# Kernel optimization log

Measured on AMD Instinct MI355X. Metric: run time of the kernel, lower is better.

## Reference

```python
import jax, jax.numpy as jnp
import numpy as np

DIM = 512
HEADS = 8
HEAD_DIM = DIM // HEADS
WIN = 7
GC = DIM // 4
EPS = 1e-5


def dwconv1d(x, w, b):
    # x: (B, Cg, L), w: (Cg, 1, k) depthwise, b: (Cg,)
    k = w.shape[-1]
    out = jax.lax.conv_general_dilated(
        x, w, window_strides=(1,), padding=[(k // 2, k // 2)],
        dimension_numbers=("NCH", "OIH", "NCH"), feature_group_count=x.shape[1])
    return out + b[None, :, None]


def group_norm(x, groups, w, b):
    # x: (B, C, *spatial); normalize over (C//groups, *spatial) per group
    shp = x.shape
    xg = x.reshape(shp[0], groups, -1)
    mu = xg.mean(-1, keepdims=True)
    var = xg.var(-1, keepdims=True)
    xn = ((xg - mu) / jnp.sqrt(var + EPS)).reshape(shp)
    bshape = (1, shp[1]) + (1,) * (x.ndim - 2)
    return xn * w.reshape(bshape) + b.reshape(bshape)


def setup_inputs() -> dict:
    key = jax.random.key(0)
    ks = jax.random.split(key, 16)
    inp = {
        "x": jax.random.normal(ks[0], (32, DIM, 56, 56), dtype=jnp.float32),
        "w3": jax.random.normal(ks[1], (GC, 1, 3), dtype=jnp.float32) * 0.2,
        "b3": jax.random.normal(ks[2], (GC,), dtype=jnp.float32) * 0.02,
        "w5": jax.random.normal(ks[3], (GC, 1, 5), dtype=jnp.float32) * 0.2,
        "b5": jax.random.normal(ks[4], (GC,), dtype=jnp.float32) * 0.02,
        "w7": jax.random.normal(ks[5], (GC, 1, 7), dtype=jnp.float32) * 0.2,
        "b7": jax.random.normal(ks[6], (GC,), dtype=jnp.float32) * 0.02,
        "w9": jax.random.normal(ks[7], (GC, 1, 9), dtype=jnp.float32) * 0.2,
        "b9": jax.random.normal(ks[8], (GC,), dtype=jnp.float32) * 0.02,
        "gnh_w": jnp.ones((DIM,), jnp.float32),
        "gnh_b": jnp.zeros((DIM,), jnp.float32),
        "gnw_w": jnp.ones((DIM,), jnp.float32),
        "gnw_b": jnp.zeros((DIM,), jnp.float32),
        "gn_w": jnp.ones((DIM,), jnp.float32),
        "gn_b": jnp.zeros((DIM,), jnp.float32),
        "qw": jax.random.normal(ks[9], (DIM,), dtype=jnp.float32) * 0.2,
        "kw": jax.random.normal(ks[10], (DIM,), dtype=jnp.float32) * 0.2,
        "vw": jax.random.normal(ks[11], (DIM,), dtype=jnp.float32) * 0.2,
    }
    return inp


def reference(x, w3, b3, w5, b5, w7, b7, w9, b9,
              gnh_w, gnh_b, gnw_w, gnw_b, gn_w, gn_b, qw, kw, vw):
    B, C, H, W = x.shape
    ws = [(w3, b3), (w5, b5), (w7, b7), (w9, b9)]

    def multi_dwc(xp):  # xp: (B, C, L)
        parts = jnp.split(xp, 4, axis=1)
        return jnp.concatenate([dwconv1d(p, w, b) for p, (w, b) in zip(parts, ws)], axis=1)

    x_h = x.mean(axis=3)  # (B, C, H)
    x_w = x.mean(axis=2)  # (B, C, W)
    x_h_attn = jax.nn.sigmoid(group_norm(multi_dwc(x_h), 4, gnh_w, gnh_b))  # (B,C,H)
    x_w_attn = jax.nn.sigmoid(group_norm(multi_dwc(x_w), 4, gnw_w, gnw_b))  # (B,C,W)
    xg = x * x_h_attn[:, :, :, None] * x_w_attn[:, :, None, :]

    # avg-pool downsample by window_size
    hh, ww = H // WIN, W // WIN
    y = xg.reshape(B, C, hh, WIN, ww, WIN).mean(axis=(3, 5))  # (B,C,hh,ww)
    y = group_norm(y, 1, gn_w, gn_b)

    L = hh * ww
    q = (y * qw[None, :, None, None]).reshape(B, HEADS, HEAD_DIM, L)
    k = (y * kw[None, :, None, None]).reshape(B, HEADS, HEAD_DIM, L)
    v = (y * vw[None, :, None, None]).reshape(B, HEADS, HEAD_DIM, L)

    scaler = HEAD_DIM ** -0.5
    attn = jnp.einsum("bhdl,bhel->bhde", q, k) * scaler  # (B,H,d,d) channel attention
    attn = jax.nn.softmax(attn, axis=-1)
    out = jnp.einsum("bhde,bhel->bhdl", attn, v)  # (B,H,d,L)
    out = out.reshape(B, C, hh, ww)

    ca = jax.nn.sigmoid(out.mean(axis=(2, 3), keepdims=True))  # (B,C,1,1)
    return ca * xg
```

## Files before the change

kernel.cpp:

```cpp
#include <hip/hip_runtime.h>
#include <math.h>

#define B_     32
#define C_     512
#define HW_    56
#define PLANE  3136
#define PLANE4 784
#define GC_    128
#define L2_    64
#define HD_    64
#define EPS_   1e-5f

typedef float floatx4 __attribute__((ext_vector_type(4)));
typedef float floatx2 __attribute__((ext_vector_type(2)));

__global__ __launch_bounds__(256) void k_means(const float* __restrict__ x,
                                               float* __restrict__ xh,
                                               float* __restrict__ xw) {
    const int bc = blockIdx.x;
    const int t  = threadIdx.x;
    __shared__ float lds[PLANE];
    __shared__ float rp[224];
    __shared__ float cp[224];

    const floatx4* p4 = (const floatx4*)(x + (size_t)bc * PLANE);
    for (int f = t; f < PLANE4; f += 256) {
        floatx4 v = p4[f];
        int base = f * 4;
        lds[base]   = v.x; lds[base+1] = v.y;
        lds[base+2] = v.z; lds[base+3] = v.w;
    }
    __syncthreads();
    if (t < 224) {
        int r = t >> 2, q = t & 3;
        float s = 0.f;
        int base = r * HW_ + q * 14;
        #pragma unroll
        for (int i = 0; i < 14; i++) s += lds[base + i];
        rp[t] = s;
        float s2 = 0.f;
        int cbase = q * 14 * HW_ + r;
        #pragma unroll
        for (int i = 0; i < 14; i++) s2 += lds[cbase + i * HW_];
        cp[t] = s2;
    }
    __syncthreads();
    if (t < HW_) {
        float rs = rp[4*t] + rp[4*t+1] + rp[4*t+2] + rp[4*t+3];
        xh[(size_t)bc * HW_ + t] = rs * (1.0f / HW_);
        float cs = cp[4*t] + cp[4*t+1] + cp[4*t+2] + cp[4*t+3];
        xw[(size_t)bc * HW_ + t] = cs * (1.0f / HW_);
    }
}

__global__ __launch_bounds__(256) void k_conv_gn_sig(
    const float* __restrict__ xh, const float* __restrict__ xw,
    const float* __restrict__ w3, const float* __restrict__ b3,
    const float* __restrict__ w5, const float* __restrict__ b5,
    const float* __restrict__ w7, const float* __restrict__ b7,
    const float* __restrict__ w9, const float* __restrict__ b9,
    const float* __restrict__ gnh_w, const float* __restrict__ gnh_b,
    const float* __restrict__ gnw_w, const float* __restrict__ gnw_b,
    float* __restrict__ ah, float* __restrict__ aw) {

    const int blk = blockIdx.x;
    const int b = blk >> 3;
    const int which = (blk & 7) >> 2;
    const int g = blk & 3;
    const int t = threadIdx.x;

    const float* in  = (which ? xw : xh) + ((size_t)(b * C_ + g * GC_)) * HW_;
    float*       out = (which ? aw : ah) + ((size_t)(b * C_ + g * GC_)) * HW_;
    const float* gw  = (which ? gnw_w : gnh_w) + g * GC_;
    const float* gb  = (which ? gnw_b : gnh_b) + g * GC_;

    const float* wsel; const float* bsel; int ks;
    switch (g) {
        case 0:  wsel = w3; bsel = b3; ks = 3; break;
        case 1:  wsel = w5; bsel = b5; ks = 5; break;
        case 2:  wsel = w7; bsel = b7; ks = 7; break;
        default: wsel = w9; bsel = b9; ks = 9; break;
    }

    __shared__ __align__(16) float lin[GC_ * HW_];
    __shared__ float wl[GC_ * 9];
    __shared__ float bl[GC_];
    __shared__ float red[10];

    {
        const floatx4* in4 = (const floatx4*)in;
        floatx4* lin4 = (floatx4*)lin;
        for (int i = t; i < GC_ * HW_ / 4; i += 256) lin4[i] = in4[i];
    }
    const int nw = GC_ * ks;
    for (int i = t; i < nw; i += 256) wl[i] = wsel[i];
    if (t < GC_) bl[t] = bsel[t];
    __syncthreads();

    const int k2 = ks >> 1;
    float acc[28];
    float s = 0.f, s2 = 0.f;
    #pragma unroll
    for (int k = 0; k < 28; k++) {
        int idx = t + k * 256;
        int c = idx / HW_, l = idx - c * HW_;
        float a = bl[c];
        for (int tt = 0; tt < ks; tt++) {
            int pos = l + tt - k2;
            if (pos >= 0 && pos < HW_) a += wl[c * ks + tt] * lin[c * HW_ + pos];
        }
        acc[k] = a;
        s += a; s2 += a * a;
    }
    #pragma unroll
    for (int o = 32; o > 0; o >>= 1) { s += __shfl_down(s, o); s2 += __shfl_down(s2, o); }
    int lane = t & 63, wid = t >> 6;
    if (lane == 0) { red[wid] = s; red[4 + wid] = s2; }
    __syncthreads();
    if (t == 0) {
        float S  = red[0] + red[1] + red[2] + red[3];
        float S2 = red[4] + red[5] + red[6] + red[7];
        float mean = S * (1.0f / (GC_ * HW_));
        float var  = S2 * (1.0f / (GC_ * HW_)) - mean * mean;
        red[8] = mean;
        red[9] = rsqrtf(var + EPS_);
    }
    __syncthreads();
    const float mean = red[8], rstd = red[9];

    #pragma unroll
    for (int k = 0; k < 28; k++) {
        int idx = t + k * 256;
        int c = idx / HW_;
        float v = (acc[k] - mean) * rstd * gw[c] + gb[c];
        out[idx] = 1.0f / (1.0f + expf(-v));
    }
}

__global__ __launch_bounds__(256) void k_pool(const float* __restrict__ x,
                                              const float* __restrict__ ah,
                                              const float* __restrict__ aw,
                                              float* __restrict__ y,
                                              floatx2* __restrict__ psum) {
    const int bc = blockIdx.x;
    const int t  = threadIdx.x;
    __shared__ float lds[PLANE];
    __shared__ float a_h[HW_];
    __shared__ float a_w[HW_];

    if (t < HW_) {
        a_h[t] = ah[(size_t)bc * HW_ + t];
        a_w[t] = aw[(size_t)bc * HW_ + t];
    }
    const floatx4* p4 = (const floatx4*)(x + (size_t)bc * PLANE);
    for (int f = t; f < PLANE4; f += 256) {
        floatx4 v = p4[f];
        int base = f * 4;
        lds[base]   = v.x; lds[base+1] = v.y;
        lds[base+2] = v.z; lds[base+3] = v.w;
    }
    __syncthreads();
    if (t < L2_) {
        int hh = t >> 3, ww = t & 7;
        float s = 0.f;
        #pragma unroll
        for (int i = 0; i < 7; i++) {
            float rsum = 0.f;
            int rbase = (7*hh + i) * HW_ + 7*ww;
            #pragma unroll
            for (int j = 0; j < 7; j++) rsum += lds[rbase + j] * a_w[7*ww + j];
            s += rsum * a_h[7*hh + i];
        }
        float ps = s * (1.0f / 49.0f);
        y[(size_t)bc * L2_ + t] = ps;
        float a = ps, a2 = ps * ps;
        #pragma unroll
        for (int off = 32; off > 0; off >>= 1) {
            a  += __shfl_down(a, off);
            a2 += __shfl_down(a2, off);
        }
        if (t == 0) {
            floatx2 pv; pv.x = a; pv.y = a2;
            psum[bc] = pv;
        }
    }
}

__global__ __launch_bounds__(256) void k_attn(const float* __restrict__ y,
                                              const floatx2* __restrict__ psum,
                                              const float* __restrict__ gn_w,
                                              const float* __restrict__ gn_b,
                                              const float* __restrict__ qw,
                                              const float* __restrict__ kw,
                                              const float* __restrict__ vw,
                                              float* __restrict__ ca) {
    const int blk = blockIdx.x;
    const int b = blk >> 3, h = blk & 7;
    const int t = threadIdx.x;

    __shared__ float yn[HD_ * 68];
    __shared__ float vbar[HD_];
    __shared__ float red[10];

    {
        floatx2 p0 = psum[b * C_ + t];
        floatx2 p1 = psum[b * C_ + 256 + t];
        float s  = p0.x + p1.x;
        float s2 = p0.y + p1.y;
        #pragma unroll
        for (int off = 32; off > 0; off >>= 1) {
            s  += __shfl_down(s, off);
            s2 += __shfl_down(s2, off);
        }
        int lane = t & 63, wid = t >> 6;
        if (lane == 0) { red[wid] = s; red[4 + wid] = s2; }
        __syncthreads();
        if (t == 0) {
            float S  = red[0] + red[1] + red[2] + red[3];
            float S2 = red[4] + red[5] + red[6] + red[7];
            float mean = S * (1.0f / (C_ * L2_));
            float var  = S2 * (1.0f / (C_ * L2_)) - mean * mean;
            red[8] = mean;
            red[9] = rsqrtf(var + EPS_);
        }
        __syncthreads();
    }
    const float mu = red[8], rstd = red[9];

    const floatx4* yp4 = (const floatx4*)(y + ((size_t)(b * C_ + h * HD_)) * L2_);
    for (int f = t; f < 1024; f += 256) {
        int d = f >> 4, lb = (f & 15) << 2;
        int ch = h * HD_ + d;
        float gsc = gn_w[ch] * rstd;
        float gof = gn_b[ch] - mu * gsc;
        floatx4 v = yp4[f];
        yn[d*68 + lb]   = v.x * gsc + gof;
        yn[d*68 + lb+1] = v.y * gsc + gof;
        yn[d*68 + lb+2] = v.z * gsc + gof;
        yn[d*68 + lb+3] = v.w * gsc + gof;
    }
    __syncthreads();

    if (t < HD_) {
        int ch = h * HD_ + t;
        float s = 0.f;
        #pragma unroll
        for (int l = 0; l < L2_; l++) s += yn[t*68 + l];
        vbar[t] = s * (1.0f / L2_) * vw[ch];
    }
    __syncthreads();

    const int d = t >> 2, eb = t & 3;
    const int ch0 = h * HD_;
    float acc[16];
    #pragma unroll
    for (int i = 0; i < 16; i++) acc[i] = 0.f;
    #pragma unroll 4
    for (int lb = 0; lb < 16; lb++) {
        floatx4 qv = *(const floatx4*)&yn[d*68 + lb*4];
        #pragma unroll
        for (int i = 0; i < 16; i++) {
            floatx4 kv = *(const floatx4*)&yn[(eb + 4*i)*68 + lb*4];
            acc[i] += qv.x*kv.x + qv.y*kv.y + qv.z*kv.z + qv.w*kv.w;
        }
    }
    const float qg = qw[ch0 + d] * 0.125f;
    float m = -1e30f;
    #pragma unroll
    for (int i = 0; i < 16; i++) {
        acc[i] *= qg * kw[ch0 + eb + 4*i];
        m = fmaxf(m, acc[i]);
    }
    m = fmaxf(m, __shfl_xor(m, 1));
    m = fmaxf(m, __shfl_xor(m, 2));
    float s1 = 0.f, s2 = 0.f;
    #pragma unroll
    for (int i = 0; i < 16; i++) {
        float p = expf(acc[i] - m);
        s1 += p;
        s2 += p * vbar[eb + 4*i];
    }
    s1 += __shfl_xor(s1, 1); s2 += __shfl_xor(s2, 1);
    s1 += __shfl_xor(s1, 2); s2 += __shfl_xor(s2, 2);
    if (eb == 0) {
        float o = s2 / s1;
        ca[(size_t)b * C_ + ch0 + d] = 1.0f / (1.0f + expf(-o));
    }
}

__global__ __launch_bounds__(256) void k_out(const float* __restrict__ x,
                                             const float* __restrict__ ah,
                                             const float* __restrict__ aw,
                                             const float* __restrict__ ca,
                                             float* __restrict__ out) {
    const unsigned total4 = (unsigned)B_ * C_ * PLANE4;
    const unsigned stride = gridDim.x * blockDim.x;
    const floatx4* px = (const floatx4*)x;
    floatx4*       po = (floatx4*)out;

    for (unsigned i = blockIdx.x * blockDim.x + threadIdx.x; i < total4; i += stride) {
        unsigned bc = i / PLANE4;
        unsigned r  = i - bc * PLANE4;
        unsigned hh = r / 14;
        unsigned jb = (r - hh * 14) * 4;

        floatx4 v  = px[i];
        floatx4 w4 = *(const floatx4*)&aw[bc * HW_ + jb];
        float   m  = ca[bc] * ah[bc * HW_ + hh];
        v.x *= m * w4.x;
        v.y *= m * w4.y;
        v.z *= m * w4.z;
        v.w *= m * w4.w;
        __builtin_nontemporal_store(v, &po[i]);
    }
}

extern "C" void kernel_launch(void* const* d_in, const int* in_sizes, int n_in,
                              void* d_out, int out_size, void* d_ws, size_t ws_size,
                              hipStream_t stream) {
    const float* x     = (const float*)d_in[0];
    const float* w3    = (const float*)d_in[1];
    const float* b3    = (const float*)d_in[2];
    const float* w5    = (const float*)d_in[3];
    const float* b5    = (const float*)d_in[4];
    const float* w7    = (const float*)d_in[5];
    const float* b7    = (const float*)d_in[6];
    const float* w9    = (const float*)d_in[7];
    const float* b9    = (const float*)d_in[8];
    const float* gnh_w = (const float*)d_in[9];
    const float* gnh_b = (const float*)d_in[10];
    const float* gnw_w = (const float*)d_in[11];
    const float* gnw_b = (const float*)d_in[12];
    const float* gn_w  = (const float*)d_in[13];
    const float* gn_b  = (const float*)d_in[14];
    const float* qw    = (const float*)d_in[15];
    const float* kw    = (const float*)d_in[16];
    const float* vw    = (const float*)d_in[17];

    float* ws = (float*)d_ws;
    const size_t N_BC56 = (size_t)B_ * C_ * HW_;
    float* xh    = ws;
    float* xw_   = xh + N_BC56;
    float* ah    = xw_ + N_BC56;
    float* aw    = ah + N_BC56;
    float* yy    = aw + N_BC56;
    float* ca    = yy + (size_t)B_ * C_ * L2_;
    floatx2* psum = (floatx2*)(ca + (size_t)B_ * C_);

    const int nbc = B_ * C_;

    k_means<<<nbc, 256, 0, stream>>>(x, xh, xw_);
    k_conv_gn_sig<<<B_ * 8, 256, 0, stream>>>(xh, xw_, w3, b3, w5, b5, w7, b7, w9, b9,
                                              gnh_w, gnh_b, gnw_w, gnw_b, ah, aw);
    k_pool<<<nbc, 256, 0, stream>>>(x, ah, aw, yy, psum);
    k_attn<<<B_ * 8, 256, 0, stream>>>(yy, psum, gn_w, gn_b, qw, kw, vw, ca);
    k_out<<<2048, 256, 0, stream>>>(x, ah, aw, ca, (float*)d_out);
}
```

Measured before the change: 170.1 us.

## Fuse depthwise conv into means kernel and group-norm sigmoid into pool kernel

The separate conv+groupnorm+sigmoid kernel is removed. Each per-(b,c) means block now computes the depthwise conv on its own row and column means and writes per-channel partial sums. The pool kernel reduces those partials across the 128-channel group, then applies the normalization and sigmoid to form its gates. This drops one launch and the low-parallelism 256-block conv kernel. In exchange, every pool block redundantly re-reduces 256 group partials and adds an extra sync.

```diff
diff --git a/kernel.cpp b/kernel.cpp
--- a/kernel.cpp
+++ b/kernel.cpp
@@ -10,18 +10,31 @@
 #define L2_    64
 #define HD_    64
 #define EPS_   1e-5f
+#define NBC    (B_*C_)
 
 typedef float floatx4 __attribute__((ext_vector_type(4)));
 typedef float floatx2 __attribute__((ext_vector_type(2)));
 
-__global__ __launch_bounds__(256) void k_means(const float* __restrict__ x,
-                                               float* __restrict__ xh,
-                                               float* __restrict__ xw) {
+__global__ __launch_bounds__(256) void k_means_conv(
+    const float* __restrict__ x,
+    const float* __restrict__ w3, const float* __restrict__ b3,
+    const float* __restrict__ w5, const float* __restrict__ b5,
+    const float* __restrict__ w7, const float* __restrict__ b7,
+    const float* __restrict__ w9, const float* __restrict__ b9,
+    float* __restrict__ ch, float* __restrict__ cw,
+    floatx2* __restrict__ pstat) {
+
     const int bc = blockIdx.x;
     const int t  = threadIdx.x;
+    const int c  = bc & (C_ - 1);
+    const int g  = c >> 7;
+    const int cc = c & (GC_ - 1);
+
     __shared__ float lds[PLANE];
     __shared__ float rp[224];
     __shared__ float cp[224];
+    __shared__ float mh[HW_];
+    __shared__ float mw[HW_];
 
     const floatx4* p4 = (const floatx4*)(x + (size_t)bc * PLANE);
     for (int f = t; f < PLANE4; f += 256) {
@@ -46,33 +59,10 @@
     }
     __syncthreads();
     if (t < HW_) {
-        float rs = rp[4*t] + rp[4*t+1] + rp[4*t+2] + rp[4*t+3];
-        xh[(size_t)bc * HW_ + t] = rs * (1.0f / HW_);
-        float cs = cp[4*t] + cp[4*t+1] + cp[4*t+2] + cp[4*t+3];
-        xw[(size_t)bc * HW_ + t] = cs * (1.0f / HW_);
-    }
-}
-
-__global__ __launch_bounds__(256) void k_conv_gn_sig(
-    const float* __restrict__ xh, const float* __restrict__ xw,
-    const float* __restrict__ w3, const float* __restrict__ b3,
-    const float* __restrict__ w5, const float* __restrict__ b5,
-    const float* __restrict__ w7, const float* __restrict__ b7,
-    const float* __restrict__ w9, const float* __restrict__ b9,
-    const float* __restrict__ gnh_w, const float* __restrict__ gnh_b,
-    const float* __restrict__ gnw_w, const float* __restrict__ gnw_b,
-    float* __restrict__ ah, float* __restrict__ aw) {
-
-    const int blk = blockIdx.x;
-    const int b = blk >> 3;
-    const int which = (blk & 7) >> 2;
-    const int g = blk & 3;
-    const int t = threadIdx.x;
-
-    const float* in  = (which ? xw : xh) + ((size_t)(b * C_ + g * GC_)) * HW_;
-    float*       out = (which ? aw : ah) + ((size_t)(b * C_ + g * GC_)) * HW_;
-    const float* gw  = (which ? gnw_w : gnh_w) + g * GC_;
-    const float* gb  = (which ? gnw_b : gnh_b) + g * GC_;
+        mh[t] = (rp[4*t] + rp[4*t+1] + rp[4*t+2] + rp[4*t+3]) * (1.0f / HW_);
+        mw[t] = (cp[4*t] + cp[4*t+1] + cp[4*t+2] + cp[4*t+3]) * (1.0f / HW_);
+    }
+    __syncthreads();
 
     const float* wsel; const float* bsel; int ks;
     switch (g) {
@@ -81,77 +71,68 @@
         case 2:  wsel = w7; bsel = b7; ks = 7; break;
         default: wsel = w9; bsel = b9; ks = 9; break;
     }
-
-    __shared__ __align__(16) float lin[GC_ * HW_];
-    __shared__ float wl[GC_ * 9];
-    __shared__ float bl[GC_];
-    __shared__ float red[10];
-
-    {
-        const floatx4* in4 = (const floatx4*)in;
-        floatx4* lin4 = (floatx4*)lin;
-        for (int i = t; i < GC_ * HW_ / 4; i += 256) lin4[i] = in4[i];
-    }
-    const int nw = GC_ * ks;
-    for (int i = t; i < nw; i += 256) wl[i] = wsel[i];
-    if (t < GC_) bl[t] = bsel[t];
-    __syncthreads();
-
     const int k2 = ks >> 1;
-    float acc[28];
-    float s = 0.f, s2 = 0.f;
-    #pragma unroll
-    for (int k = 0; k < 28; k++) {
-        int idx = t + k * 256;
-        int c = idx / HW_, l = idx - c * HW_;
-        float a = bl[c];
+    const int lane = t & 63, wid = t >> 6;
+
+    float cv = 0.f;
+    bool valid = (wid < 2) && (lane < HW_);
+    if (valid) {
+        const float* m = (wid == 0) ? mh : mw;
+        float a = bsel[cc];
         for (int tt = 0; tt < ks; tt++) {
-            int pos = l + tt - k2;
-            if (pos >= 0 && pos < HW_) a += wl[c * ks + tt] * lin[c * HW_ + pos];
-        }
-        acc[k] = a;
-        s += a; s2 += a * a;
-    }
-    #pragma unroll
-    for (int o = 32; o > 0; o >>= 1) { s += __shfl_down(s, o); s2 += __shfl_down(s2, o); }
-    int lane = t & 63, wid = t >> 6;
-    if (lane == 0) { red[wid] = s; red[4 + wid] = s2; }
-    __syncthreads();
-    if (t == 0) {
-        float S  = red[0] + red[1] + red[2] + red[3];
-        float S2 = red[4] + red[5] + red[6] + red[7];
-        float mean = S * (1.0f / (GC_ * HW_));
-        float var  = S2 * (1.0f / (GC_ * HW_)) - mean * mean;
-        red[8] = mean;
-        red[9] = rsqrtf(var + EPS_);
-    }
-    __syncthreads();
-    const float mean = red[8], rstd = red[9];
-
-    #pragma unroll
-    for (int k = 0; k < 28; k++) {
-        int idx = t + k * 256;
-        int c = idx / HW_;
-        float v = (acc[k] - mean) * rstd * gw[c] + gb[c];
-        out[idx] = 1.0f / (1.0f + expf(-v));
-    }
-}
-
-__global__ __launch_bounds__(256) void k_pool(const float* __restrict__ x,
-                                              const float* __restrict__ ah,
-                                              const float* __restrict__ aw,
-                                              float* __restrict__ y,
-                                              floatx2* __restrict__ psum) {
+            int pos = lane + tt - k2;
+            if (pos >= 0 && pos < HW_) a += wsel[cc * ks + tt] * m[pos];
+        }
+        cv = a;
+        float* o = (wid == 0) ? ch : cw;
+        o[(size_t)bc * HW_ + lane] = a;
+    }
+    if (wid < 2) {
+        float s = cv, s2 = cv * cv;
+        #pragma unroll
+        for (int off = 32; off > 0; off >>= 1) {
+            s  += __shfl_down(s, off);
+            s2 += __shfl_down(s2, off);
+        }
+        if (lane == 0) {
+            floatx2 pv; pv.x = s; pv.y = s2;
+            pstat[(size_t)wid * NBC + bc] = pv;
+        }
+    }
+}
+
+__global__ __launch_bounds__(256) void k_pool(
+    const float* __restrict__ x,
+    const float* __restrict__ ch, const float* __restrict__ cw,
+    const floatx2* __restrict__ pstat,
+    const float* __restrict__ gnh_w, const float* __restrict__ gnh_b,
+    const float* __restrict__ gnw_w, const float* __restrict__ gnw_b,
+    float* __restrict__ ah, float* __restrict__ aw,
+    float* __restrict__ y, floatx2* __restrict__ psum) {
+
     const int bc = blockIdx.x;
     const int t  = threadIdx.x;
+    const int b  = bc >> 9;
+    const int c  = bc & (C_ - 1);
+    const int g  = c >> 7;
+    const int gbase = b * C_ + g * GC_;
+
     __shared__ float lds[PLANE];
     __shared__ float a_h[HW_];
     __shared__ float a_w[HW_];
-
-    if (t < HW_) {
-        a_h[t] = ah[(size_t)bc * HW_ + t];
-        a_w[t] = aw[(size_t)bc * HW_ + t];
-    }
+    __shared__ float red[4];
+
+    const int lane = t & 63, wid = t >> 6;
+
+    float ps = 0.f, ps2 = 0.f;
+    if (wid < 2) {
+        const floatx2* P = pstat + (size_t)wid * NBC + gbase;
+        floatx2 p0 = P[lane];
+        floatx2 p1 = P[64 + lane];
+        ps  = p0.x + p1.x;
+        ps2 = p0.y + p1.y;
+    }
+
     const floatx4* p4 = (const floatx4*)(x + (size_t)bc * PLANE);
     for (int f = t; f < PLANE4; f += 256) {
         floatx4 v = p4[f];
@@ -159,7 +140,39 @@
         lds[base]   = v.x; lds[base+1] = v.y;
         lds[base+2] = v.z; lds[base+3] = v.w;
     }
-    __syncthreads();
+
+    if (wid < 2) {
+        #pragma unroll
+        for (int off = 32; off > 0; off >>= 1) {
+            ps  += __shfl_down(ps, off);
+            ps2 += __shfl_down(ps2, off);
+        }
+        if (lane == 0) { red[wid * 2] = ps; red[wid * 2 + 1] = ps2; }
+    }
+    __syncthreads();
+
+    {
+        const float inv_n = 1.0f / (GC_ * HW_);
+        if (wid == 0 && lane < HW_) {
+            float mean = red[0] * inv_n;
+            float var  = red[1] * inv_n - mean * mean;
+            float rstd = rsqrtf(var + EPS_);
+            float v = (ch[(size_t)bc * HW_ + lane] - mean) * rstd * gnh_w[c] + gnh_b[c];
+            float gate = 1.0f / (1.0f + expf(-v));
+            a_h[lane] = gate;
+            ah[(size_t)bc * HW_ + lane] = gate;
+        } else if (wid == 1 && lane < HW_) {
+            float mean = red[2] * inv_n;
+            float var  = red[3] * inv_n - mean * mean;
+            float rstd = rsqrtf(var + EPS_);
+            float v = (cw[(size_t)bc * HW_ + lane] - mean) * rstd * gnw_w[c] + gnw_b[c];
+            float gate = 1.0f / (1.0f + expf(-v));
+            a_w[lane] = gate;
+            aw[(size_t)bc * HW_ + lane] = gate;
+        }
+    }
+    __syncthreads();
+
     if (t < L2_) {
         int hh = t >> 3, ww = t & 7;
         float s = 0.f;
@@ -171,17 +184,17 @@
             for (int j = 0; j < 7; j++) rsum += lds[rbase + j] * a_w[7*ww + j];
             s += rsum * a_h[7*hh + i];
         }
-        float ps = s * (1.0f / 49.0f);
-        y[(size_t)bc * L2_ + t] = ps;
-        float a = ps, a2 = ps * ps;
+        float pv = s * (1.0f / 49.0f);
+        y[(size_t)bc * L2_ + t] = pv;
+        float a = pv, a2 = pv * pv;
         #pragma unroll
         for (int off = 32; off > 0; off >>= 1) {
             a  += __shfl_down(a, off);
             a2 += __shfl_down(a2, off);
         }
         if (t == 0) {
-            floatx2 pv; pv.x = a; pv.y = a2;
-            psum[bc] = pv;
+            floatx2 q; q.x = a; q.y = a2;
+            psum[bc] = q;
         }
     }
 }
@@ -230,9 +243,9 @@
     const floatx4* yp4 = (const floatx4*)(y + ((size_t)(b * C_ + h * HD_)) * L2_);
     for (int f = t; f < 1024; f += 256) {
         int d = f >> 4, lb = (f & 15) << 2;
-        int ch = h * HD_ + d;
-        float gsc = gn_w[ch] * rstd;
-        float gof = gn_b[ch] - mu * gsc;
+        int chn = h * HD_ + d;
+        float gsc = gn_w[chn] * rstd;
+        float gof = gn_b[chn] - mu * gsc;
         floatx4 v = yp4[f];
         yn[d*68 + lb]   = v.x * gsc + gof;
         yn[d*68 + lb+1] = v.y * gsc + gof;
@@ -242,11 +255,11 @@
     __syncthreads();
 
     if (t < HD_) {
-        int ch = h * HD_ + t;
+        int chn = h * HD_ + t;
         float s = 0.f;
         #pragma unroll
         for (int l = 0; l < L2_; l++) s += yn[t*68 + l];
-        vbar[t] = s * (1.0f / L2_) * vw[ch];
+        vbar[t] = s * (1.0f / L2_) * vw[chn];
     }
     __syncthreads();
 
@@ -339,20 +352,20 @@
 
     float* ws = (float*)d_ws;
     const size_t N_BC56 = (size_t)B_ * C_ * HW_;
-    float* xh    = ws;
-    float* xw_   = xh + N_BC56;
-    float* ah    = xw_ + N_BC56;
+    float* ch    = ws;
+    float* cw    = ch + N_BC56;
+    float* ah    = cw + N_BC56;
     float* aw    = ah + N_BC56;
     float* yy    = aw + N_BC56;
     float* ca    = yy + (size_t)B_ * C_ * L2_;
-    floatx2* psum = (floatx2*)(ca + (size_t)B_ * C_);
-
-    const int nbc = B_ * C_;
-
-    k_means<<<nbc, 256, 0, stream>>>(x, xh, xw_);
-    k_conv_gn_sig<<<B_ * 8, 256, 0, stream>>>(xh, xw_, w3, b3, w5, b5, w7, b7, w9, b9,
-                                              gnh_w, gnh_b, gnw_w, gnw_b, ah, aw);
-    k_pool<<<nbc, 256, 0, stream>>>(x, ah, aw, yy, psum);
+    floatx2* psum  = (floatx2*)(ca + (size_t)B_ * C_);
+    floatx2* pstat = psum + NBC;
+
+    k_means_conv<<<NBC, 256, 0, stream>>>(x, w3, b3, w5, b5, w7, b7, w9, b9,
+                                          ch, cw, pstat);
+    k_pool<<<NBC, 256, 0, stream>>>(x, ch, cw, pstat,
+                                    gnh_w, gnh_b, gnw_w, gnw_b,
+                                    ah, aw, yy, psum);
     k_attn<<<B_ * 8, 256, 0, stream>>>(yy, psum, gn_w, gn_b, qw, kw, vw, ca);
     k_out<<<2048, 256, 0, stream>>>(x, ah, aw, ca, (float*)d_out);
 }
```

After: 147.8 us, median of 2. 1.15x faster.
